# Optimization experiments

Hardware: AMD Instinct MI355X
Metric: run time of the kernel (lower is better)

Reference implementation:

```python
import jax, jax.numpy as jnp
import numpy as np

NUM_E = 1024        # codebook size
E_DIM = 256         # embedding dim (== channels of x)
BETA = 0.25

def setup_inputs() -> dict:
    key = jax.random.key(0)
    kx, kw = jax.random.split(key)
    x = jax.random.normal(kx, (16, E_DIM, 64, 64), dtype=jnp.float32)
    # embedding weight init: uniform(-1/num_e, 1/e_dim), matching torch init
    codebook = jax.random.uniform(kw, (NUM_E, E_DIM), dtype=jnp.float32,
                                  minval=-1.0 / NUM_E, maxval=1.0 / E_DIM)
    return {"x": x, "codebook": codebook}

def reference(x, codebook):
    beta = BETA
    # NCHW -> NHWC, flatten to [N, D]
    xp = jnp.transpose(x, (0, 2, 3, 1))          # [B,H,W,D]
    x_shape = xp.shape
    xf = xp.reshape(-1, E_DIM)                   # [N,D]
    cb_sq = jnp.sum(codebook ** 2, axis=1)                 # [K]
    in_sq = jnp.sum(xf ** 2, axis=1, keepdims=True)        # [N,1]
    dist = in_sq + cb_sq - 2.0 * (xf @ codebook.T)         # [N,K]
    idx = jnp.argmin(dist, axis=1)                         # [N]
    # one-hot encodings (returned like the torch module)
    encodings = jax.nn.one_hot(idx, NUM_E, dtype=jnp.float32)  # [N,K]
    # one-hot @ codebook == gather; use gather (same math, no big GEMM)
    xq = jnp.take(codebook, idx, axis=0).reshape(x_shape)      # [B,H,W,D]
    embedding_loss = jnp.mean((jax.lax.stop_gradient(xq) - xp) ** 2)
    quantization_loss = jnp.mean((xq - jax.lax.stop_gradient(xp)) ** 2)
    loss = quantization_loss + beta * embedding_loss
    e_mean = jnp.mean(encodings, axis=0)
    # NOTE: original code uses +1e10 inside the log (likely a typo for 1e-10);
    # we reproduce it faithfully.
    perplexity = jnp.exp(-jnp.sum(e_mean * jnp.log(e_mean + 10000000000.0)))
    # straight-through estimator
    xq_st = xp + jax.lax.stop_gradient(xq - xp)
    xq_out = jnp.transpose(xq_st, (0, 3, 1, 2))  # NHWC -> NCHW
    return (loss, xq_out, perplexity, encodings)
```

## Files before the change

kernel.cpp:

```cpp
#include <hip/hip_runtime.h>
#include <math.h>
#include <stdint.h>

typedef float f4u __attribute__((ext_vector_type(4), aligned(4)));
typedef unsigned int u4v __attribute__((ext_vector_type(4)));
typedef __attribute__((ext_vector_type(8))) short short8;
typedef __attribute__((ext_vector_type(4))) float float4v;

#define DIM 256
#define KCB 1024
#define PERP_OFF 16777217
#define ENC_OFF  16777218
#define CAP 32
#define EPS 0.008f
#define NPB 128
#define SCORE_BLOCKS 512

__device__ __forceinline__ float np_sumsq128(const float* a, int stride) {
  float r[8];
  #pragma unroll
  for (int j = 0; j < 8; ++j) { float v = a[j * stride]; r[j] = __fmul_rn(v, v); }
  #pragma unroll
  for (int i = 8; i < 128; i += 8) {
    #pragma unroll
    for (int j = 0; j < 8; ++j) {
      float v = a[(i + j) * stride];
      r[j] = __fadd_rn(r[j], __fmul_rn(v, v));
    }
  }
  float s01 = __fadd_rn(r[0], r[1]);
  float s23 = __fadd_rn(r[2], r[3]);
  float s45 = __fadd_rn(r[4], r[5]);
  float s67 = __fadd_rn(r[6], r[7]);
  return __fadd_rn(__fadd_rn(s01, s23), __fadd_rn(s45, s67));
}

__device__ __forceinline__ unsigned short f2bf(float f) {
  unsigned u = __float_as_uint(f);
  u += 0x7FFFu + ((u >> 16) & 1u);
  return (unsigned short)(u >> 16);
}

__global__ __launch_bounds__(64)
void k_prep(const float* __restrict__ cb, unsigned short* __restrict__ e_bf16,
            float* __restrict__ cb_sq, int* __restrict__ counts) {
  const int k = blockIdx.x;
  const int l = threadIdx.x;
  float4 v = ((const float4*)(cb + k * DIM))[l];
  unsigned short bs[4] = {f2bf(v.x), f2bf(v.y), f2bf(v.z), f2bf(v.w)};
  *(ushort4*)(e_bf16 + k * DIM + l * 4) = *(ushort4*)bs;
  if (l == 0) {
    const float* p = cb + k * DIM;
    cb_sq[k] = __fadd_rn(np_sumsq128(p, 1), np_sumsq128(p + 128, 1));
    counts[k] = 0;
  }
}

__global__ __launch_bounds__(256, 3)
void k_score(const float* __restrict__ x, const unsigned short* __restrict__ e_bf16,
             const float* __restrict__ cb_sq, unsigned int* __restrict__ gcnt,
             unsigned short* __restrict__ glist) {
  __shared__ unsigned int   lcnt[NPB];
  __shared__ unsigned short llist[NPB * CAP];
  __shared__ float          lsc[NPB * CAP];
  __shared__ float          lmin[NPB];
  const int t    = threadIdx.x;
  const int wv   = t >> 6;
  const int lane = t & 63;
  const int l15  = lane & 15;
  const int quad = lane >> 4;
  if (t < NPB) lcnt[t] = 0;
  __syncthreads();

  short8 Bf[2][8];
  const int nbase = blockIdx.x * NPB + wv * 32;
  #pragma unroll
  for (int g = 0; g < 2; ++g) {
    const int n = nbase + g * 16 + l15;
    const float* xb = x + (n >> 12) * 1048576 + (n & 4095);
    #pragma unroll
    for (int ks = 0; ks < 8; ++ks) {
      const int d0 = ks * 32 + quad * 8;
      union { unsigned short s[8]; short8 v; } u;
      #pragma unroll
      for (int j = 0; j < 8; ++j) u.s[j] = f2bf(xb[(d0 + j) * 4096]);
      Bf[g][ks] = u.v;
    }
  }

  float m[2] = {1e30f, 1e30f};
  for (int ct = 0; ct < 64; ++ct) {
    float4v acc[2];
    #pragma unroll
    for (int g = 0; g < 2; ++g) acc[g] = (float4v){0.f, 0.f, 0.f, 0.f};
    const unsigned short* ap = e_bf16 + (ct * 16 + l15) * DIM + quad * 8;
    #pragma unroll
    for (int ks = 0; ks < 8; ++ks) {
      const short8 a = *(const short8*)(ap + ks * 32);
      #pragma unroll
      for (int g = 0; g < 2; ++g)
        acc[g] = __builtin_amdgcn_mfma_f32_16x16x32_bf16(a, Bf[g][ks], acc[g], 0, 0, 0);
    }
    const float4 cs = *(const float4*)(cb_sq + ct * 16 + quad * 4);
    #pragma unroll
    for (int g = 0; g < 2; ++g) {
      const float sa[4] = {fmaf(-2.f, acc[g].x, cs.x), fmaf(-2.f, acc[g].y, cs.y),
                           fmaf(-2.f, acc[g].z, cs.z), fmaf(-2.f, acc[g].w, cs.w)};
      float bm = fminf(fminf(sa[0], sa[1]), fminf(sa[2], sa[3]));
      bm = fminf(bm, m[g]);
      bm = fminf(bm, __shfl_xor(bm, 16));
      bm = fminf(bm, __shfl_xor(bm, 32));
      m[g] = bm;
      const float thr = bm + EPS;
      const float sblk = fminf(fminf(sa[0], sa[1]), fminf(sa[2], sa[3]));
      if (sblk <= thr) {
        const int nl = wv * 32 + g * 16 + l15;
        #pragma unroll
        for (int r = 0; r < 4; ++r) {
          if (sa[r] <= thr) {
            unsigned slot = atomicAdd(&lcnt[nl], 1u);
            if (slot < CAP) {
              llist[nl * CAP + slot] = (unsigned short)(ct * 16 + quad * 4 + r);
              lsc[nl * CAP + slot]   = sa[r];
            }
          }
        }
      }
    }
  }
  if (quad == 0) {
    #pragma unroll
    for (int g = 0; g < 2; ++g) lmin[wv * 32 + g * 16 + l15] = m[g];
  }
  __syncthreads();

  if (t < NPB) {
    const unsigned cnt = lcnt[t];
    unsigned outc = cnt;
    if (cnt <= CAP) {
      const float thrf = lmin[t] + EPS;
      unsigned j = 0;
      for (unsigned i = 0; i < cnt; ++i) {
        const unsigned short c = llist[t * CAP + i];
        if (lsc[t * CAP + i] <= thrf) llist[t * CAP + j++] = c;
      }
      outc = j;
    }
    gcnt[blockIdx.x * NPB + t] = outc;

    u4v* gdst = (u4v*)(glist + (size_t)blockIdx.x * NPB * CAP);
    const u4v* lsrc = (const u4v*)llist;
    #pragma unroll
    for (int j = 0; j < 4; ++j)
      __builtin_nontemporal_store(lsrc[t * 4 + j], gdst + t * 4 + j);
  }
}

__global__ __launch_bounds__(256)
void k_fused(const float* __restrict__ x, const float* __restrict__ cb,
             const float* __restrict__ cb_sq,
             const unsigned int* __restrict__ gcnt,
             const unsigned short* __restrict__ glist,
             float* __restrict__ out1, float* __restrict__ enc,
             int* __restrict__ counts, double* __restrict__ partials) {
  const int t  = threadIdx.x;
  const int bh = blockIdx.x;
  const int b  = bh >> 6, h = bh & 63;
  __shared__ float isq_s[64];
  __shared__ int   idxs[64];

  if (t < 64) {
    const int n = bh * 64 + t;
    const float* p = x + b * 1048576 + (n & 4095);
    float h0 = np_sumsq128(p, 4096);
    float h1 = np_sumsq128(p + 128 * 4096, 4096);
    isq_s[t] = __fadd_rn(h0, h1);
  }
  __syncthreads();

  {
    const int nl = t >> 2;
    const int q  = t & 3;
    const int n  = bh * 64 + nl;
    const unsigned cnt = gcnt[n];
    const float* xb = x + b * 1048576 + (n & 4095);
    const float isq = isq_s[nl];
    float bv = 1e30f; int bc = 0x7FFFFFFF;

    if (cnt <= CAP) {
      const unsigned short* lst = glist + (size_t)n * CAP;
      for (unsigned i = q; i < cnt; i += 4) {
        const int c1 = lst[i];
        const float4* e1 = (const float4*)(cb + c1 * DIM);
        float d1 = 0.f;
        #pragma unroll 4
        for (int qq = 0; qq < 64; ++qq) {
          const float4 a = e1[qq];
          d1 = fmaf(xb[(qq * 4 + 0) * 4096], a.x, d1);
          d1 = fmaf(xb[(qq * 4 + 1) * 4096], a.y, d1);
          d1 = fmaf(xb[(qq * 4 + 2) * 4096], a.z, d1);
          d1 = fmaf(xb[(qq * 4 + 3) * 4096], a.w, d1);
        }
        const float dist = __fsub_rn(__fadd_rn(isq, cb_sq[c1]), __fmul_rn(2.f, d1));
        if (dist < bv || (dist == bv && c1 < bc)) { bv = dist; bc = c1; }
      }
    } else {
      for (int c = q; c < KCB; c += 4) {
        const float4* e1 = (const float4*)(cb + c * DIM);
        float d1 = 0.f;
        #pragma unroll 4
        for (int qq = 0; qq < 64; ++qq) {
          const float4 a = e1[qq];
          d1 = fmaf(xb[(qq * 4 + 0) * 4096], a.x, d1);
          d1 = fmaf(xb[(qq * 4 + 1) * 4096], a.y, d1);
          d1 = fmaf(xb[(qq * 4 + 2) * 4096], a.z, d1);
          d1 = fmaf(xb[(qq * 4 + 3) * 4096], a.w, d1);
        }
        const float dist = __fsub_rn(__fadd_rn(isq, cb_sq[c]), __fmul_rn(2.f, d1));
        if (dist < bv || (dist == bv && c < bc)) { bv = dist; bc = c; }
      }
    }
    {
      float ov = __shfl_xor(bv, 1); int oc = __shfl_xor(bc, 1);
      if (ov < bv || (ov == bv && oc < bc)) { bv = ov; bc = oc; }
      ov = __shfl_xor(bv, 2); oc = __shfl_xor(bc, 2);
      if (ov < bv || (ov == bv && oc < bc)) { bv = ov; bc = oc; }
    }
    if (q == 0) { idxs[nl] = bc; atomicAdd(counts + bc, 1); }
  }
  __syncthreads();

  {
    float* base = enc + (size_t)bh * 65536 + t * 4;
    #pragma unroll 8
    for (int r = 0; r < 64; ++r) {
      const int bi = idxs[r];
      f4u v = {0.f, 0.f, 0.f, 0.f};
      if ((bi >> 2) == t) {
        if ((bi & 3) == 0) v.x = 1.f; else if ((bi & 3) == 1) v.y = 1.f;
        else if ((bi & 3) == 2) v.z = 1.f; else v.w = 1.f;
      }
      __builtin_nontemporal_store(v, (f4u*)(base + r * 1024));
    }
  }

  const int w4 = (t & 15) * 4;
  const int cg = t >> 4;
  float qf[4][16];
  #pragma unroll
  for (int i = 0; i < 4; ++i) {
    const float4* rp = (const float4*)(cb + idxs[w4 + i] * DIM + cg * 16);
    #pragma unroll
    for (int jq = 0; jq < 4; ++jq) {
      const float4 v = rp[jq];
      qf[i][jq * 4 + 0] = v.x; qf[i][jq * 4 + 1] = v.y;
      qf[i][jq * 4 + 2] = v.z; qf[i][jq * 4 + 3] = v.w;
    }
  }

  double s = 0.0;
  #pragma unroll
  for (int j = 0; j < 16; ++j) {
    const int c = cg * 16 + j;
    const size_t off = ((size_t)b << 20) + ((size_t)c << 12) + (h << 6) + w4;
    const float4 xp = *(const float4*)(x + off);
    const float q0 = qf[0][j], q1 = qf[1][j], q2 = qf[2][j], q3 = qf[3][j];
    const float d0 = __fsub_rn(q0, xp.x), d1 = __fsub_rn(q1, xp.y);
    const float d2 = __fsub_rn(q2, xp.z), d3 = __fsub_rn(q3, xp.w);
    f4u o;
    o.x = __fadd_rn(xp.x, d0); o.y = __fadd_rn(xp.y, d1);
    o.z = __fadd_rn(xp.z, d2); o.w = __fadd_rn(xp.w, d3);
    __builtin_nontemporal_store(o, (f4u*)(out1 + off));
    s += (double)(d0*d0) + (double)(d1*d1) + (double)(d2*d2) + (double)(d3*d3);
  }
  #pragma unroll
  for (int off = 32; off > 0; off >>= 1) s += __shfl_down(s, off);
  __shared__ double sm[4];
  if ((t & 63) == 0) sm[t >> 6] = s;
  __syncthreads();
  if (t == 0) partials[bh] = (sm[0] + sm[1]) + (sm[2] + sm[3]);
}

__global__ __launch_bounds__(256)
void k_final(const double* __restrict__ partials, const int* __restrict__ counts,
             float* __restrict__ out) {
  const int t = threadIdx.x;
  double s = 0.0;
  #pragma unroll
  for (int i = 0; i < 4; ++i) s += partials[t + i * 256];
  #pragma unroll
  for (int off = 32; off > 0; off >>= 1) s += __shfl_down(s, off);
  __shared__ double sm[4];
  __shared__ float smf[4];
  if ((t & 63) == 0) sm[t >> 6] = s;

  float ps = 0.f;
  #pragma unroll
  for (int i = 0; i < 4; ++i) {
    const float p = (float)counts[t + i * 256] * (1.0f / 65536.0f);
    ps += p * logf(1.0e10f + p);
  }
  #pragma unroll
  for (int off = 32; off > 0; off >>= 1) ps += __shfl_down(ps, off);
  if ((t & 63) == 0) smf[t >> 6] = ps;
  __syncthreads();
  if (t == 0) {
    const double tot = (sm[0] + sm[1]) + (sm[2] + sm[3]);
    const float mval = (float)(tot / 16777216.0);
    out[0] = mval + 0.25f * mval;
    out[PERP_OFF] = expf(-((smf[0] + smf[1]) + (smf[2] + smf[3])));
  }
}

extern "C" void kernel_launch(void* const* d_in, const int* in_sizes, int n_in,
                              void* d_out, int out_size, void* d_ws, size_t ws_size,
                              hipStream_t stream) {
  const float* x  = (const float*)d_in[0];
  const float* cb = (const float*)d_in[1];
  float* out = (float*)d_out;
  char*  ws  = (char*)d_ws;

  int*            counts   = (int*)(ws + 0);
  float*          cb_sq    = (float*)(ws + 4096);
  double*         partials = (double*)(ws + 532480);
  unsigned short* e_bf16   = (unsigned short*)(ws + 1589248);
  unsigned int*   gcnt     = (unsigned int*)(ws + 2113536);
  unsigned short* glist    = (unsigned short*)(ws + 2375680);

  k_prep  <<<1024, 64, 0, stream>>>(cb, e_bf16, cb_sq, counts);
  k_score <<<SCORE_BLOCKS, 256, 0, stream>>>(x, e_bf16, cb_sq, gcnt, glist);
  k_fused <<<1024, 256, 0, stream>>>(x, cb, cb_sq, gcnt, glist, out + 1,
                                     out + ENC_OFF, counts, partials);
  k_final <<<1, 256, 0, stream>>>(partials, counts, out);
}
```

Measured before the change: 597.1 us.

## Fuse scoring and refinement/output kernels into one mega kernel using shared candidate lists

Merges the bf16 MFMA scoring kernel with the fp32 refinement, one-hot, straight-through output and loss kernel so candidate lists and counts stay in shared memory instead of going through global memory. Each block now handles 128 pixels, so the refinement uses 2 threads per pixel instead of 4, and the output phase loops over two 64-pixel rows. The input-norm computation is done by the idle upper half of the threads during candidate filtering. This removes a kernel launch and the global list round-trip, at the cost of halving refinement parallelism and running the whole pipeline on only 512 blocks with the heavy register limit of the scoring kernel.

```diff
diff --git a/kernel.cpp b/kernel.cpp
--- a/kernel.cpp
+++ b/kernel.cpp
@@ -3,7 +3,6 @@
 #include <stdint.h>
 
 typedef float f4u __attribute__((ext_vector_type(4), aligned(4)));
-typedef unsigned int u4v __attribute__((ext_vector_type(4)));
 typedef __attribute__((ext_vector_type(8))) short short8;
 typedef __attribute__((ext_vector_type(4))) float float4v;
 
@@ -14,7 +13,7 @@
 #define CAP 32
 #define EPS 0.008f
 #define NPB 128
-#define SCORE_BLOCKS 512
+#define MEGA_BLOCKS 512
 
 __device__ __forceinline__ float np_sumsq128(const float* a, int stride) {
   float r[8];
@@ -57,23 +56,30 @@
 }
 
 __global__ __launch_bounds__(256, 3)
-void k_score(const float* __restrict__ x, const unsigned short* __restrict__ e_bf16,
-             const float* __restrict__ cb_sq, unsigned int* __restrict__ gcnt,
-             unsigned short* __restrict__ glist) {
+void k_mega(const float* __restrict__ x, const float* __restrict__ cb,
+            const unsigned short* __restrict__ e_bf16,
+            const float* __restrict__ cb_sq,
+            float* __restrict__ out1, float* __restrict__ enc,
+            int* __restrict__ counts, double* __restrict__ partials) {
   __shared__ unsigned int   lcnt[NPB];
   __shared__ unsigned short llist[NPB * CAP];
   __shared__ float          lsc[NPB * CAP];
   __shared__ float          lmin[NPB];
+  __shared__ float          isq_s[NPB];
+  __shared__ int            idxs[NPB];
+  __shared__ double         sm[4];
+
   const int t    = threadIdx.x;
   const int wv   = t >> 6;
   const int lane = t & 63;
   const int l15  = lane & 15;
   const int quad = lane >> 4;
+  const int blk  = blockIdx.x;
   if (t < NPB) lcnt[t] = 0;
   __syncthreads();
 
   short8 Bf[2][8];
-  const int nbase = blockIdx.x * NPB + wv * 32;
+  const int nbase = blk * NPB + wv * 32;
   #pragma unroll
   for (int g = 0; g < 2; ++g) {
     const int n = nbase + g * 16 + l15;
@@ -146,50 +152,29 @@
       }
       outc = j;
     }
-    gcnt[blockIdx.x * NPB + t] = outc;
-
-    u4v* gdst = (u4v*)(glist + (size_t)blockIdx.x * NPB * CAP);
-    const u4v* lsrc = (const u4v*)llist;
-    #pragma unroll
-    for (int j = 0; j < 4; ++j)
-      __builtin_nontemporal_store(lsrc[t * 4 + j], gdst + t * 4 + j);
-  }
-}
-
-__global__ __launch_bounds__(256)
-void k_fused(const float* __restrict__ x, const float* __restrict__ cb,
-             const float* __restrict__ cb_sq,
-             const unsigned int* __restrict__ gcnt,
-             const unsigned short* __restrict__ glist,
-             float* __restrict__ out1, float* __restrict__ enc,
-             int* __restrict__ counts, double* __restrict__ partials) {
-  const int t  = threadIdx.x;
-  const int bh = blockIdx.x;
-  const int b  = bh >> 6, h = bh & 63;
-  __shared__ float isq_s[64];
-  __shared__ int   idxs[64];
-
-  if (t < 64) {
-    const int n = bh * 64 + t;
-    const float* p = x + b * 1048576 + (n & 4095);
+    lcnt[t] = outc;
+  } else {
+    const int tt = t - NPB;
+    const int n  = blk * NPB + tt;
+    const float* p = x + (n >> 12) * 1048576 + (n & 4095);
     float h0 = np_sumsq128(p, 4096);
     float h1 = np_sumsq128(p + 128 * 4096, 4096);
-    isq_s[t] = __fadd_rn(h0, h1);
+    isq_s[tt] = __fadd_rn(h0, h1);
   }
   __syncthreads();
 
   {
-    const int nl = t >> 2;
-    const int q  = t & 3;
-    const int n  = bh * 64 + nl;
-    const unsigned cnt = gcnt[n];
-    const float* xb = x + b * 1048576 + (n & 4095);
+    const int nl = t >> 1;
+    const int q  = t & 1;
+    const int n  = blk * NPB + nl;
+    const unsigned cnt = lcnt[nl];
+    const float* xb = x + (n >> 12) * 1048576 + (n & 4095);
     const float isq = isq_s[nl];
     float bv = 1e30f; int bc = 0x7FFFFFFF;
 
     if (cnt <= CAP) {
-      const unsigned short* lst = glist + (size_t)n * CAP;
-      for (unsigned i = q; i < cnt; i += 4) {
+      const unsigned short* lst = llist + nl * CAP;
+      for (unsigned i = q; i < cnt; i += 2) {
         const int c1 = lst[i];
         const float4* e1 = (const float4*)(cb + c1 * DIM);
         float d1 = 0.f;
@@ -205,7 +190,7 @@
         if (dist < bv || (dist == bv && c1 < bc)) { bv = dist; bc = c1; }
       }
     } else {
-      for (int c = q; c < KCB; c += 4) {
+      for (int c = q; c < KCB; c += 2) {
         const float4* e1 = (const float4*)(cb + c * DIM);
         float d1 = 0.f;
         #pragma unroll 4
@@ -221,64 +206,69 @@
       }
     }
     {
-      float ov = __shfl_xor(bv, 1); int oc = __shfl_xor(bc, 1);
+      const float ov = __shfl_xor(bv, 1); const int oc = __shfl_xor(bc, 1);
       if (ov < bv || (ov == bv && oc < bc)) { bv = ov; bc = oc; }
-      ov = __shfl_xor(bv, 2); oc = __shfl_xor(bc, 2);
-      if (ov < bv || (ov == bv && oc < bc)) { bv = ov; bc = oc; }
     }
     if (q == 0) { idxs[nl] = bc; atomicAdd(counts + bc, 1); }
   }
   __syncthreads();
-
-  {
-    float* base = enc + (size_t)bh * 65536 + t * 4;
-    #pragma unroll 8
-    for (int r = 0; r < 64; ++r) {
-      const int bi = idxs[r];
-      f4u v = {0.f, 0.f, 0.f, 0.f};
-      if ((bi >> 2) == t) {
-        if ((bi & 3) == 0) v.x = 1.f; else if ((bi & 3) == 1) v.y = 1.f;
-        else if ((bi & 3) == 2) v.z = 1.f; else v.w = 1.f;
-      }
-      __builtin_nontemporal_store(v, (f4u*)(base + r * 1024));
-    }
-  }
 
   const int w4 = (t & 15) * 4;
   const int cg = t >> 4;
-  float qf[4][16];
-  #pragma unroll
-  for (int i = 0; i < 4; ++i) {
-    const float4* rp = (const float4*)(cb + idxs[w4 + i] * DIM + cg * 16);
-    #pragma unroll
-    for (int jq = 0; jq < 4; ++jq) {
-      const float4 v = rp[jq];
-      qf[i][jq * 4 + 0] = v.x; qf[i][jq * 4 + 1] = v.y;
-      qf[i][jq * 4 + 2] = v.z; qf[i][jq * 4 + 3] = v.w;
-    }
-  }
-
-  double s = 0.0;
-  #pragma unroll
-  for (int j = 0; j < 16; ++j) {
-    const int c = cg * 16 + j;
-    const size_t off = ((size_t)b << 20) + ((size_t)c << 12) + (h << 6) + w4;
-    const float4 xp = *(const float4*)(x + off);
-    const float q0 = qf[0][j], q1 = qf[1][j], q2 = qf[2][j], q3 = qf[3][j];
-    const float d0 = __fsub_rn(q0, xp.x), d1 = __fsub_rn(q1, xp.y);
-    const float d2 = __fsub_rn(q2, xp.z), d3 = __fsub_rn(q3, xp.w);
-    f4u o;
-    o.x = __fadd_rn(xp.x, d0); o.y = __fadd_rn(xp.y, d1);
-    o.z = __fadd_rn(xp.z, d2); o.w = __fadd_rn(xp.w, d3);
-    __builtin_nontemporal_store(o, (f4u*)(out1 + off));
-    s += (double)(d0*d0) + (double)(d1*d1) + (double)(d2*d2) + (double)(d3*d3);
-  }
-  #pragma unroll
-  for (int off = 32; off > 0; off >>= 1) s += __shfl_down(s, off);
-  __shared__ double sm[4];
-  if ((t & 63) == 0) sm[t >> 6] = s;
-  __syncthreads();
-  if (t == 0) partials[bh] = (sm[0] + sm[1]) + (sm[2] + sm[3]);
+  #pragma unroll
+  for (int half = 0; half < 2; ++half) {
+    const int bh = blk * 2 + half;
+    const int b  = bh >> 6, h = bh & 63;
+    const int* idx_h = idxs + half * 64;
+
+    {
+      float* base = enc + (size_t)bh * 65536 + t * 4;
+      #pragma unroll 8
+      for (int r = 0; r < 64; ++r) {
+        const int bi = idx_h[r];
+        f4u v = {0.f, 0.f, 0.f, 0.f};
+        if ((bi >> 2) == t) {
+          if ((bi & 3) == 0) v.x = 1.f; else if ((bi & 3) == 1) v.y = 1.f;
+          else if ((bi & 3) == 2) v.z = 1.f; else v.w = 1.f;
+        }
+        __builtin_nontemporal_store(v, (f4u*)(base + r * 1024));
+      }
+    }
+
+    float qf[4][16];
+    #pragma unroll
+    for (int i = 0; i < 4; ++i) {
+      const float4* rp = (const float4*)(cb + idx_h[w4 + i] * DIM + cg * 16);
+      #pragma unroll
+      for (int jq = 0; jq < 4; ++jq) {
+        const float4 v = rp[jq];
+        qf[i][jq * 4 + 0] = v.x; qf[i][jq * 4 + 1] = v.y;
+        qf[i][jq * 4 + 2] = v.z; qf[i][jq * 4 + 3] = v.w;
+      }
+    }
+
+    double s = 0.0;
+    #pragma unroll
+    for (int j = 0; j < 16; ++j) {
+      const int c = cg * 16 + j;
+      const size_t off = ((size_t)b << 20) + ((size_t)c << 12) + (h << 6) + w4;
+      const float4 xp = *(const float4*)(x + off);
+      const float q0 = qf[0][j], q1 = qf[1][j], q2 = qf[2][j], q3 = qf[3][j];
+      const float d0 = __fsub_rn(q0, xp.x), d1 = __fsub_rn(q1, xp.y);
+      const float d2 = __fsub_rn(q2, xp.z), d3 = __fsub_rn(q3, xp.w);
+      f4u o;
+      o.x = __fadd_rn(xp.x, d0); o.y = __fadd_rn(xp.y, d1);
+      o.z = __fadd_rn(xp.z, d2); o.w = __fadd_rn(xp.w, d3);
+      __builtin_nontemporal_store(o, (f4u*)(out1 + off));
+      s += (double)(d0*d0) + (double)(d1*d1) + (double)(d2*d2) + (double)(d3*d3);
+    }
+    #pragma unroll
+    for (int off = 32; off > 0; off >>= 1) s += __shfl_down(s, off);
+    if ((t & 63) == 0) sm[t >> 6] = s;
+    __syncthreads();
+    if (t == 0) partials[bh] = (sm[0] + sm[1]) + (sm[2] + sm[3]);
+    __syncthreads();
+  }
 }
 
 __global__ __launch_bounds__(256)
@@ -322,14 +312,11 @@
 
   int*            counts   = (int*)(ws + 0);
   float*          cb_sq    = (float*)(ws + 4096);
-  double*         partials = (double*)(ws + 532480);
-  unsigned short* e_bf16   = (unsigned short*)(ws + 1589248);
-  unsigned int*   gcnt     = (unsigned int*)(ws + 2113536);
-  unsigned short* glist    = (unsigned short*)(ws + 2375680);
-
-  k_prep  <<<1024, 64, 0, stream>>>(cb, e_bf16, cb_sq, counts);
-  k_score <<<SCORE_BLOCKS, 256, 0, stream>>>(x, e_bf16, cb_sq, gcnt, glist);
-  k_fused <<<1024, 256, 0, stream>>>(x, cb, cb_sq, gcnt, glist, out + 1,
-                                     out + ENC_OFF, counts, partials);
-  k_final <<<1, 256, 0, stream>>>(partials, counts, out);
-}
+  double*         partials = (double*)(ws + 8192);
+  unsigned short* e_bf16   = (unsigned short*)(ws + 16384);
+
+  k_prep <<<1024, 64, 0, stream>>>(cb, e_bf16, cb_sq, counts);
+  k_mega <<<MEGA_BLOCKS, 256, 0, stream>>>(x, cb, e_bf16, cb_sq, out + 1,
+                                           out + ENC_OFF, counts, partials);
+  k_final<<<1, 256, 0, stream>>>(partials, counts, out);
+}
```

Measured after the change: 598.4 us. Within noise of the previous version (+0.2%).

## Stage codebook tiles in double-buffered LDS and batch running-min reductions in scoring kernel

Applied to the files above, without the earlier changes.

The scoring kernel now cooperatively loads each 16-row bf16 codebook tile into XOR-swizzled shared memory with double buffering, instead of each wave reading codebook fragments directly from global memory. The cross-lane min/threshold shuffle reduction now runs every iteration only for the first four tiles, then once every four tiles, which cuts shuffles but loosens the candidate threshold. The fused kernel also splits the per-row squared-norm computation across 128 threads rather than 64, and the workspace offsets are compacted. The new shared buffers and a barrier every iteration raise LDS use and add sync cost, which may lower occupancy. A looser threshold may also let more candidates through.

```diff
diff --git a/kernel.cpp b/kernel.cpp
--- a/kernel.cpp
+++ b/kernel.cpp
@@ -60,20 +60,28 @@
 void k_score(const float* __restrict__ x, const unsigned short* __restrict__ e_bf16,
              const float* __restrict__ cb_sq, unsigned int* __restrict__ gcnt,
              unsigned short* __restrict__ glist) {
+  __shared__ unsigned short As[2][16 * 256];
   __shared__ unsigned int   lcnt[NPB];
   __shared__ unsigned short llist[NPB * CAP];
   __shared__ float          lsc[NPB * CAP];
   __shared__ float          lmin[NPB];
+
   const int t    = threadIdx.x;
   const int wv   = t >> 6;
   const int lane = t & 63;
   const int l15  = lane & 15;
   const int quad = lane >> 4;
+  const int blk  = blockIdx.x;
   if (t < NPB) lcnt[t] = 0;
-  __syncthreads();
+
+  const int srow = t >> 4;
+  const int scol = (t & 15) * 16;
+  const int ssw  = (srow & 7) << 3;
+  const int dst0 = srow * 256 + (scol ^ ssw);
+  const int dst1 = srow * 256 + ((scol + 8) ^ ssw);
 
   short8 Bf[2][8];
-  const int nbase = blockIdx.x * NPB + wv * 32;
+  const int nbase = blk * NPB + wv * 32;
   #pragma unroll
   for (int g = 0; g < 2; ++g) {
     const int n = nbase + g * 16 + l15;
@@ -88,36 +96,56 @@
     }
   }
 
-  float m[2] = {1e30f, 1e30f};
+  {
+    const u4v* g0 = (const u4v*)(e_bf16 + t * 16);
+    const u4v v0 = g0[0], v1 = g0[1];
+    *(u4v*)(As[0] + dst0) = v0;
+    *(u4v*)(As[0] + dst1) = v1;
+  }
+  __syncthreads();
+
+  float mlane[2] = {1e30f, 1e30f};
+  float thr[2]   = {1e30f, 1e30f};
+  float mfin[2]  = {1e30f, 1e30f};
   for (int ct = 0; ct < 64; ++ct) {
+    const int p = ct & 1;
+    u4v n0, n1;
+    const bool havenext = (ct < 63);
+    if (havenext) {
+      const u4v* gn = (const u4v*)(e_bf16 + (ct + 1) * 4096 + t * 16);
+      n0 = gn[0]; n1 = gn[1];
+    }
     float4v acc[2];
-    #pragma unroll
-    for (int g = 0; g < 2; ++g) acc[g] = (float4v){0.f, 0.f, 0.f, 0.f};
-    const unsigned short* ap = e_bf16 + (ct * 16 + l15) * DIM + quad * 8;
+    acc[0] = (float4v){0.f, 0.f, 0.f, 0.f};
+    acc[1] = (float4v){0.f, 0.f, 0.f, 0.f};
+    const unsigned short* base = As[p] + l15 * 256;
+    const int rsw = (l15 & 7) << 3;
     #pragma unroll
     for (int ks = 0; ks < 8; ++ks) {
-      const short8 a = *(const short8*)(ap + ks * 32);
-      #pragma unroll
-      for (int g = 0; g < 2; ++g)
-        acc[g] = __builtin_amdgcn_mfma_f32_16x16x32_bf16(a, Bf[g][ks], acc[g], 0, 0, 0);
+      const int u = (quad * 8 + ks * 32) ^ rsw;
+      const short8 a = *(const short8*)(base + u);
+      acc[0] = __builtin_amdgcn_mfma_f32_16x16x32_bf16(a, Bf[0][ks], acc[0], 0, 0, 0);
+      acc[1] = __builtin_amdgcn_mfma_f32_16x16x32_bf16(a, Bf[1][ks], acc[1], 0, 0, 0);
     }
     const float4 cs = *(const float4*)(cb_sq + ct * 16 + quad * 4);
     #pragma unroll
     for (int g = 0; g < 2; ++g) {
-      const float sa[4] = {fmaf(-2.f, acc[g].x, cs.x), fmaf(-2.f, acc[g].y, cs.y),
-                           fmaf(-2.f, acc[g].z, cs.z), fmaf(-2.f, acc[g].w, cs.w)};
-      float bm = fminf(fminf(sa[0], sa[1]), fminf(sa[2], sa[3]));
-      bm = fminf(bm, m[g]);
-      bm = fminf(bm, __shfl_xor(bm, 16));
-      bm = fminf(bm, __shfl_xor(bm, 32));
-      m[g] = bm;
-      const float thr = bm + EPS;
-      const float sblk = fminf(fminf(sa[0], sa[1]), fminf(sa[2], sa[3]));
-      if (sblk <= thr) {
+      float sa[4];
+      sa[0] = fmaf(-2.f, acc[g].x, cs.x); sa[1] = fmaf(-2.f, acc[g].y, cs.y);
+      sa[2] = fmaf(-2.f, acc[g].z, cs.z); sa[3] = fmaf(-2.f, acc[g].w, cs.w);
+      const float cmin = fminf(fminf(sa[0], sa[1]), fminf(sa[2], sa[3]));
+      mlane[g] = fminf(mlane[g], cmin);
+      if (ct < 4) {
+        float bm = fminf(mlane[g], __shfl_xor(mlane[g], 16));
+        bm = fminf(bm, __shfl_xor(bm, 32));
+        mfin[g] = bm;
+        thr[g]  = bm + EPS;
+      }
+      if (cmin <= thr[g]) {
         const int nl = wv * 32 + g * 16 + l15;
         #pragma unroll
         for (int r = 0; r < 4; ++r) {
-          if (sa[r] <= thr) {
+          if (sa[r] <= thr[g]) {
             unsigned slot = atomicAdd(&lcnt[nl], 1u);
             if (slot < CAP) {
               llist[nl * CAP + slot] = (unsigned short)(ct * 16 + quad * 4 + r);
@@ -127,10 +155,24 @@
         }
       }
     }
+    if (ct >= 4 && (ct & 3) == 3) {
+      #pragma unroll
+      for (int g = 0; g < 2; ++g) {
+        float bm = fminf(mlane[g], __shfl_xor(mlane[g], 16));
+        bm = fminf(bm, __shfl_xor(bm, 32));
+        mfin[g] = bm;
+        thr[g]  = bm + EPS;
+      }
+    }
+    if (havenext) {
+      *(u4v*)(As[p ^ 1] + dst0) = n0;
+      *(u4v*)(As[p ^ 1] + dst1) = n1;
+    }
+    __syncthreads();
   }
   if (quad == 0) {
     #pragma unroll
-    for (int g = 0; g < 2; ++g) lmin[wv * 32 + g * 16 + l15] = m[g];
+    for (int g = 0; g < 2; ++g) lmin[wv * 32 + g * 16 + l15] = mfin[g];
   }
   __syncthreads();
 
@@ -146,9 +188,9 @@
       }
       outc = j;
     }
-    gcnt[blockIdx.x * NPB + t] = outc;
-
-    u4v* gdst = (u4v*)(glist + (size_t)blockIdx.x * NPB * CAP);
+    gcnt[blk * NPB + t] = outc;
+
+    u4v* gdst = (u4v*)(glist + (size_t)blk * NPB * CAP);
     const u4v* lsrc = (const u4v*)llist;
     #pragma unroll
     for (int j = 0; j < 4; ++j)
@@ -166,15 +208,15 @@
   const int t  = threadIdx.x;
   const int bh = blockIdx.x;
   const int b  = bh >> 6, h = bh & 63;
-  __shared__ float isq_s[64];
+  __shared__ float hpart[128];
   __shared__ int   idxs[64];
 
-  if (t < 64) {
-    const int n = bh * 64 + t;
-    const float* p = x + b * 1048576 + (n & 4095);
-    float h0 = np_sumsq128(p, 4096);
-    float h1 = np_sumsq128(p + 128 * 4096, 4096);
-    isq_s[t] = __fadd_rn(h0, h1);
+  if (t < 128) {
+    const int nl = t >> 1;
+    const int p  = t & 1;
+    const int n  = bh * 64 + nl;
+    const float* xp = x + b * 1048576 + (n & 4095) + p * 128 * 4096;
+    hpart[t] = np_sumsq128(xp, 4096);
   }
   __syncthreads();
 
@@ -184,7 +226,7 @@
     const int n  = bh * 64 + nl;
     const unsigned cnt = gcnt[n];
     const float* xb = x + b * 1048576 + (n & 4095);
-    const float isq = isq_s[nl];
+    const float isq = __fadd_rn(hpart[2 * nl], hpart[2 * nl + 1]);
     float bv = 1e30f; int bc = 0x7FFFFFFF;
 
     if (cnt <= CAP) {
@@ -322,14 +364,14 @@
 
   int*            counts   = (int*)(ws + 0);
   float*          cb_sq    = (float*)(ws + 4096);
-  double*         partials = (double*)(ws + 532480);
-  unsigned short* e_bf16   = (unsigned short*)(ws + 1589248);
-  unsigned int*   gcnt     = (unsigned int*)(ws + 2113536);
-  unsigned short* glist    = (unsigned short*)(ws + 2375680);
-
-  k_prep  <<<1024, 64, 0, stream>>>(cb, e_bf16, cb_sq, counts);
-  k_score <<<SCORE_BLOCKS, 256, 0, stream>>>(x, e_bf16, cb_sq, gcnt, glist);
-  k_fused <<<1024, 256, 0, stream>>>(x, cb, cb_sq, gcnt, glist, out + 1,
-                                     out + ENC_OFF, counts, partials);
-  k_final <<<1, 256, 0, stream>>>(partials, counts, out);
-}
+  double*         partials = (double*)(ws + 8192);
+  unsigned short* e_bf16   = (unsigned short*)(ws + 16384);
+  unsigned int*   gcnt     = (unsigned int*)(ws + 540672);
+  unsigned short* glist    = (unsigned short*)(ws + 802816);
+
+  k_prep <<<1024, 64, 0, stream>>>(cb, e_bf16, cb_sq, counts);
+  k_score<<<SCORE_BLOCKS, 256, 0, stream>>>(x, e_bf16, cb_sq, gcnt, glist);
+  k_fused<<<1024, 256, 0, stream>>>(x, cb, cb_sq, gcnt, glist, out + 1,
+                                    out + ENC_OFF, counts, partials);
+  k_final<<<1, 256, 0, stream>>>(partials, counts, out);
+}
```

New measurement: 523.9 us. 12.3% less time.
